# Kernel tuning notes

Measured on AMD Instinct MI355X. Metric: run time of the kernel, lower is better.

Reference implementation:

```python
import jax, jax.numpy as jnp
import numpy as np

B, S, D_IN = 16, 512, 768
HID, OUT = 64, 12
NEG = 1e12


def setup_inputs() -> dict:
    key = jax.random.key(0)
    k1, k2, k3 = jax.random.split(key, 3)
    x = jax.random.normal(k1, (B, S, D_IN), dtype=jnp.float32)
    mask = jnp.ones((B, S), dtype=jnp.float32)
    W = jax.random.normal(k2, (D_IN, HID * OUT * 2), dtype=jnp.float32) * 0.02
    b = jax.random.normal(k3, (HID * OUT * 2,), dtype=jnp.float32) * 0.02
    return {"x": x, "mask": mask, "W": W, "b": b}


def reference(x, mask, W, b):
    Bb, Ss, _ = x.shape
    h, out = HID, OUT
    # QKV-style projection, split into `out` heads of 2h each
    proj = (x @ W + b).reshape(Bb, Ss, out, 2 * h)  # [b, s, out, 2h]
    qw, kw = proj[..., :h], proj[..., h:]           # [b, s, out, h]

    # Sinusoidal position embedding (merge='zero'): interleaved sin/cos
    pos_ids = jnp.arange(Ss, dtype=x.dtype)
    inv_freq = jnp.power(10000.0, -2.0 * jnp.arange(h // 2, dtype=x.dtype) / h)
    ang = pos_ids[:, None] * inv_freq               # [s, h/2]
    sin, cos = jnp.sin(ang), jnp.cos(ang)
    # torch: pos[..., None, 1::2].repeat(1,1,1,2) -> TILED (not interleaved)
    cos_pos = jnp.concatenate([cos, cos], axis=-1)[None, :, None, :]  # [1, s, 1, h]
    sin_pos = jnp.concatenate([sin, sin], axis=-1)[None, :, None, :]

    def rope(w):
        # stack([-w_odd, w_even], -1).reshape -> interleaved rotation partner
        w2 = jnp.stack([-w[..., 1::2], w[..., ::2]], axis=-1).reshape(w.shape)
        return w * cos_pos + w2 * sin_pos

    qw = rope(qw)
    kw = rope(kw)

    logits = jnp.einsum('bmhd,bnhd->bhmn', qw, kw)  # [b, out, s, s]

    pad = mask[:, None, None, :]                    # broadcast over [b, out, s, s]
    logits = logits * pad - (1.0 - pad) * NEG

    tril = jnp.tril(jnp.ones((Ss, Ss), dtype=logits.dtype), -1)
    logits = logits - tril * NEG

    return logits / (h ** 0.5)
```

## Files before the change

kernel.cpp:

```cpp
#include <hip/hip_runtime.h>
#include <stdint.h>

#define DIN   768
#define NPROJ 1536
#define SEQ   512
#define NHEAD 12
#define NBATCH 16
#define NEGV  1000000000000.0f

typedef short bf16x8 __attribute__((ext_vector_type(8)));
typedef float f32x4  __attribute__((ext_vector_type(4)));
typedef unsigned short u16x8 __attribute__((ext_vector_type(8)));

__device__ __forceinline__ unsigned short f2bf(float f) {
    union { float f; unsigned int u; } v; v.f = f;
    return (unsigned short)((v.u + 0x7FFFu + ((v.u >> 16) & 1u)) >> 16);
}
__device__ __forceinline__ float bf2f(unsigned short u) {
    union { unsigned int u; float f; } v; v.u = ((unsigned int)u) << 16;
    return v.f;
}

__device__ __forceinline__ void gl_lds16(const unsigned short* g, unsigned short* l) {
    __builtin_amdgcn_global_load_lds(
        (const __attribute__((address_space(1))) unsigned int*)(uintptr_t)g,
        (__attribute__((address_space(3))) unsigned int*)(uintptr_t)l,
        16, 0, 0);
}

__device__ __forceinline__ void stage128x64(const unsigned short* __restrict__ g,
                                            int gstride, unsigned short* lds,
                                            int w, int lane) {
#pragma unroll
    for (int t = 0; t < 4; t++) {
        int lr = w * 32 + t * 8 + (lane >> 3);
        int c16 = (lane & 7) ^ (lr & 7);
        gl_lds16(g + (size_t)lr * gstride + c16 * 8,
                 lds + (w * 32 + t * 8) * 64);
    }
}
__device__ __forceinline__ int swz(int row, int cg) {
    return row * 64 + ((cg ^ (row & 7)) << 3);
}

__global__ __launch_bounds__(256) void k_prep(const float* __restrict__ X,
                                              unsigned short* __restrict__ Xb,
                                              const float* __restrict__ W,
                                              unsigned short* __restrict__ Wt,
                                              float* __restrict__ trig) {
    __shared__ unsigned short T[64][72];
    const int bid = blockIdx.x, tid = threadIdx.x;
    if (bid < 288) {
        int n0 = (bid % 24) * 64, k0 = (bid / 24) * 64;
#pragma unroll
        for (int it = 0; it < 4; it++) {
            int c = tid + it * 256;
            int kl = c >> 4, nl = (c & 15) * 4;
            float4 v = *(const float4*)&W[(size_t)(k0 + kl) * NPROJ + n0 + nl];
            T[nl + 0][kl] = f2bf(v.x);
            T[nl + 1][kl] = f2bf(v.y);
            T[nl + 2][kl] = f2bf(v.z);
            T[nl + 3][kl] = f2bf(v.w);
        }
        __syncthreads();
#pragma unroll
        for (int it = 0; it < 2; it++) {
            int c = tid + it * 256;
            int nl = c >> 3, kb = (c & 7) * 8;
            *(int4*)&Wt[(size_t)(n0 + nl) * DIN + k0 + kb] = *(int4*)&T[nl][kb];
        }
        return;
    }
    if (bid < 352) {
        int gi = (bid - 288) * 256 + tid;
        int ss = gi >> 5, j = gi & 31;
        const float C = 0.41524101186092034f;
        float cs, sn;
        sincosf((float)ss * exp2f(-(float)j * C), &sn, &cs);
        trig[2 * gi]     = cs;
        trig[2 * gi + 1] = sn;
        return;
    }
    int i = ((bid - 352) * 256 + tid) * 4;
    float4 v = *(const float4*)&X[i];
    short4 s;
    s.x = (short)f2bf(v.x); s.y = (short)f2bf(v.y);
    s.z = (short)f2bf(v.z); s.w = (short)f2bf(v.w);
    *(short4*)&Xb[i] = s;
}

template <bool PRE>
__global__ __launch_bounds__(256) void k_gemm(const float* __restrict__ X,
                                              const unsigned short* __restrict__ Xb,
                                              const unsigned short* __restrict__ Wt,
                                              const float* __restrict__ bias,
                                              const float* __restrict__ trig,
                                              unsigned short* __restrict__ P) {
    __shared__ unsigned short smem[17408];
    unsigned short* sA = smem;
    unsigned short* sB = smem + 8192;
    const int tid = threadIdx.x;
    const int bid = blockIdx.x;
    const int xcd = bid & 7, t0 = bid >> 3;
    const int m0 = (xcd + 8 * (t0 / 12)) * 128;
    const int n0 = (t0 % 12) * 128;
    const int lane = tid & 63, w = tid >> 6;
    const int q = lane >> 4, r = lane & 15;
    const int wm = w >> 1, wn = w & 1;
    f32x4 acc[4][4];
#pragma unroll
    for (int i = 0; i < 4; i++)
#pragma unroll
        for (int j = 0; j < 4; j++) acc[i][j] = (f32x4){0.f, 0.f, 0.f, 0.f};

    const unsigned short* Ag = Xb + (size_t)m0 * DIN;
    const unsigned short* Bg = Wt + (size_t)n0 * DIN;

    for (int k0 = 0; k0 < DIN; k0 += 64) {
        __syncthreads();
        if (PRE) {
            stage128x64(Ag + k0, DIN, sA, w, lane);
        } else {
#pragma unroll
            for (int it = 0; it < 4; it++) {
                int c = tid + it * 256;
                int row = c >> 3, c16 = c & 7;
                const float* xp = &X[(size_t)(m0 + row) * DIN + k0 + c16 * 8];
                float4 v0 = *(const float4*)xp;
                float4 v1 = *(const float4*)(xp + 4);
                u16x8 sv;
                sv[0] = f2bf(v0.x); sv[1] = f2bf(v0.y);
                sv[2] = f2bf(v0.z); sv[3] = f2bf(v0.w);
                sv[4] = f2bf(v1.x); sv[5] = f2bf(v1.y);
                sv[6] = f2bf(v1.z); sv[7] = f2bf(v1.w);
                *(u16x8*)&sA[swz(row, c16)] = sv;
            }
        }
        stage128x64(Bg + k0, DIN, sB, w, lane);
        __syncthreads();
#pragma unroll
        for (int kk = 0; kk < 64; kk += 32) {
            const int cg = (kk >> 3) + q;
            bf16x8 af[4], bfr[4];
#pragma unroll
            for (int t = 0; t < 4; t++)
                af[t] = *(const bf16x8*)&sA[swz(wm * 64 + t * 16 + r, cg)];
#pragma unroll
            for (int t = 0; t < 4; t++)
                bfr[t] = *(const bf16x8*)&sB[swz(wn * 64 + t * 16 + r, cg)];
#pragma unroll
            for (int tm = 0; tm < 4; tm++)
#pragma unroll
                for (int tn = 0; tn < 4; tn++)
                    acc[tm][tn] = __builtin_amdgcn_mfma_f32_16x16x32_bf16(
                        af[tm], bfr[tn], acc[tm][tn], 0, 0, 0);
        }
    }
    float bb[4];
#pragma unroll
    for (int tn = 0; tn < 4; tn++) bb[tn] = bias[n0 + wn * 64 + tn * 16 + r];
    __syncthreads();
    unsigned short* sT = smem;
#pragma unroll
    for (int tm = 0; tm < 4; tm++) {
        int rowb = wm * 64 + tm * 16 + q * 4;
#pragma unroll
        for (int tn = 0; tn < 4; tn++) {
            int col = wn * 64 + tn * 16 + r;
#pragma unroll
            for (int i = 0; i < 4; i++)
                sT[(rowb + i) * 136 + col] = f2bf(acc[tm][tn][i] + bb[tn]);
        }
    }
    __syncthreads();
#pragma unroll
    for (int it = 0; it < 8; it++) {
        int c = tid + it * 256;
        int row = c >> 4, colb = (c & 15) * 8;
        int m = m0 + row;
        int s = m & (SEQ - 1);
        int base = colb & 31;
        union { int4 v; unsigned short u[8]; } pk;
        pk.v = *(int4*)&sT[row * 136 + colb];
        float wv[8];
#pragma unroll
        for (int j = 0; j < 8; j++) wv[j] = bf2f(pk.u[j]);
        const float* tp = &trig[2 * (s * 32 + base)];
#pragma unroll
        for (int p = 0; p < 4; p++) {
            float4 tt = *(const float4*)&tp[4 * p];
            float oe = wv[2 * p] * tt.x - wv[2 * p + 1] * tt.y;
            float oo = wv[2 * p + 1] * tt.z + wv[2 * p] * tt.w;
            pk.u[2 * p]     = f2bf(oe);
            pk.u[2 * p + 1] = f2bf(oo);
        }
        *(int4*)&P[(size_t)m * NPROJ + n0 + colb] = pk.v;
    }
}

__global__ __launch_bounds__(256, 2) void k_attn(const unsigned short* __restrict__ P,
                                                 const float* __restrict__ mask,
                                                 float* __restrict__ out) {
    __shared__ __attribute__((aligned(16))) unsigned short smem[32768];
    const int tid = threadIdx.x;
    const int bi = blockIdx.x;
    const int x  = bi & 7, s = bi >> 3;
    const int g  = x + 8 * (s >> 4);
    const int rb = s & 15;
    const int b  = g / NHEAD, h = g % NHEAD;
    const int lane = tid & 63, wn = tid >> 6;
    const int q = lane >> 4, r = lane & 15;
    const int w = wn;
    const size_t obase = ((size_t)((b * NHEAD + h) * SEQ)) * SEQ;
    const int m0 = rb * 32;

    const unsigned short* Pk = P + (size_t)b * SEQ * NPROJ + h * 128 + 64;
#pragma unroll
    for (int c = 0; c < 4; c++)
        stage128x64(Pk + (size_t)(c * 128) * NPROJ, NPROJ, smem + c * 128 * 64, w, lane);

    const unsigned short* Pq = P + (size_t)b * SEQ * NPROJ + h * 128;
    bf16x8 qf[2][2];
#pragma unroll
    for (int rt = 0; rt < 2; rt++)
#pragma unroll
        for (int x2 = 0; x2 < 2; x2++)
            qf[rt][x2] = *(const bf16x8*)
                &Pq[(size_t)(m0 + rt * 16 + r) * NPROJ + x2 * 32 + q * 8];

    f32x4 mk4[8];
#pragma unroll
    for (int t = 0; t < 8; t++)
        mk4[t] = *(const f32x4*)&mask[b * SEQ + (wn * 8 + t) * 16 + q * 4];

    f32x4 acc[8][2];
#pragma unroll
    for (int t = 0; t < 8; t++) {
        acc[t][0] = (f32x4){0.f, 0.f, 0.f, 0.f};
        acc[t][1] = (f32x4){0.f, 0.f, 0.f, 0.f};
    }

    __syncthreads();

#pragma unroll
    for (int t = 0; t < 8; t++) {
        const int ct = wn * 8 + t;
        if (ct >= 2 * rb) {
            bf16x8 kf[2];
#pragma unroll
            for (int x2 = 0; x2 < 2; x2++)
                kf[x2] = *(const bf16x8*)&smem[swz(ct * 16 + r, x2 * 4 + q)];
#pragma unroll
            for (int x2 = 0; x2 < 2; x2++) {
                acc[t][0] = __builtin_amdgcn_mfma_f32_16x16x32_bf16(
                    kf[x2], qf[0][x2], acc[t][0], 0, 0, 0);
                acc[t][1] = __builtin_amdgcn_mfma_f32_16x16x32_bf16(
                    kf[x2], qf[1][x2], acc[t][1], 0, 0, 0);
            }
        }
    }
    __syncthreads();

    float* sOut = (float*)smem;
#pragma unroll
    for (int rt = 0; rt < 2; rt++) {
        const int m = m0 + rt * 16 + r;
#pragma unroll
        for (int t = 0; t < 8; t++) {
            const int ct = wn * 8 + t;
            const int nb = ct * 16 + q * 4;
            f32x4 o;
            if (ct >= 2 * rb) {
#pragma unroll
                for (int j = 0; j < 4; j++)
                    o[j] = (acc[t][rt][j] * mk4[t][j]
                            - (1.f - mk4[t][j]) * NEGV
                            - ((nb + j) < m ? NEGV : 0.f)) * 0.125f;
            } else {
#pragma unroll
                for (int j = 0; j < 4; j++)
                    o[j] = (-(1.f - mk4[t][j]) * NEGV - NEGV) * 0.125f;
            }
            *(f32x4*)&sOut[(rt * 16 + r) * 512 + nb] = o;
        }
    }
    __syncthreads();
    float* od = out + obase + (size_t)m0 * SEQ;
#pragma unroll
    for (int it = 0; it < 16; it++) {
        const int c = tid + it * 256;
        f32x4 v = *(const f32x4*)&sOut[c * 4];
        *(f32x4*)&od[c * 4] = v;
    }
}

extern "C" void kernel_launch(void* const* d_in, const int* in_sizes, int n_in,
                              void* d_out, int out_size, void* d_ws, size_t ws_size,
                              hipStream_t stream) {
    const float* x    = (const float*)d_in[0];
    const float* mask = (const float*)d_in[1];
    const float* W    = (const float*)d_in[2];
    const float* bias = (const float*)d_in[3];
    float* out = (float*)d_out;

    const size_t wtN   = (size_t)NPROJ * DIN;
    const size_t pN    = (size_t)NBATCH * SEQ * NPROJ;
    const size_t xN    = (size_t)NBATCH * SEQ * DIN;
    const size_t trigN = (size_t)SEQ * 32 * 2;
    unsigned short* Wt = (unsigned short*)d_ws;
    unsigned short* P  = Wt + wtN;
    float* trig        = (float*)(P + pN);
    unsigned short* Xb = (unsigned short*)(trig + trigN);
    const bool pre = ws_size >= (wtN + pN + xN) * sizeof(unsigned short)
                               + trigN * sizeof(float);

    const int xblocks = (int)(xN / 1024);
    k_prep<<<pre ? (352 + xblocks) : 352, 256, 0, stream>>>(x, Xb, W, Wt, trig);
    if (pre) {
        k_gemm<true><<<dim3(768), 256, 0, stream>>>(x, Xb, Wt, bias, trig, P);
    } else {
        k_gemm<false><<<dim3(768), 256, 0, stream>>>(x, nullptr, Wt, bias, trig, P);
    }
    k_attn<<<dim3(NBATCH * NHEAD * (SEQ / 32)), 256, 0, stream>>>(P, mask, out);
}
```

Before: 278.8 us.

## Move constant lower-triangle fill into prep kernel and trim attention work

The fully masked strictly-lower-triangular output blocks, which depend only on the mask, are now written by extra blocks appended to the prep kernel. The attention kernel then stores only the upper and diagonal columns of each row block and skips staging K chunks that lie entirely below the diagonal. This takes roughly half of the output writes off the attention kernel's critical path. The cost is a larger prep grid and a variable-width store loop with integer divides.

```diff
diff --git a/kernel.cpp b/kernel.cpp
--- a/kernel.cpp
+++ b/kernel.cpp
@@ -7,6 +7,7 @@
 #define NHEAD 12
 #define NBATCH 16
 #define NEGV  1000000000000.0f
+#define NFILL 2880
 
 typedef short bf16x8 __attribute__((ext_vector_type(8)));
 typedef float f32x4  __attribute__((ext_vector_type(4)));
@@ -47,9 +48,29 @@
                                               unsigned short* __restrict__ Xb,
                                               const float* __restrict__ W,
                                               unsigned short* __restrict__ Wt,
-                                              float* __restrict__ trig) {
+                                              float* __restrict__ trig,
+                                              const float* __restrict__ mask,
+                                              float* __restrict__ out) {
     __shared__ unsigned short T[64][72];
     const int bid = blockIdx.x, tid = threadIdx.x;
+    if (bid >= (int)gridDim.x - NFILL) {
+        int f = bid - ((int)gridDim.x - NFILL);
+        int g = f / 15, rb = f % 15 + 1;
+        int b = g / NHEAD, h = g % NHEAD;
+        const int m0 = rb * 32, W4 = 8 * rb;
+        const size_t obase = ((size_t)((b * NHEAD + h) * SEQ)) * SEQ;
+        for (int i = tid; i < 32 * W4; i += 256) {
+            int row = i / W4, c4 = i - row * W4;
+            int n = c4 * 4;
+            f32x4 mk = *(const f32x4*)&mask[b * SEQ + n];
+            f32x4 o;
+#pragma unroll
+            for (int j = 0; j < 4; j++)
+                o[j] = (-(1.f - mk[j]) * NEGV - NEGV) * 0.125f;
+            *(f32x4*)&out[obase + (size_t)(m0 + row) * SEQ + n] = o;
+        }
+        return;
+    }
     if (bid < 288) {
         int n0 = (bid % 24) * 64, k0 = (bid / 24) * 64;
 #pragma unroll
@@ -217,7 +238,9 @@
     const unsigned short* Pk = P + (size_t)b * SEQ * NPROJ + h * 128 + 64;
 #pragma unroll
     for (int c = 0; c < 4; c++)
-        stage128x64(Pk + (size_t)(c * 128) * NPROJ, NPROJ, smem + c * 128 * 64, w, lane);
+        if ((c + 1) * 128 > m0)
+            stage128x64(Pk + (size_t)(c * 128) * NPROJ, NPROJ,
+                        smem + c * 128 * 64, w, lane);
 
     const unsigned short* Pq = P + (size_t)b * SEQ * NPROJ + h * 128;
     bf16x8 qf[2][2];
@@ -268,29 +291,25 @@
 #pragma unroll
         for (int t = 0; t < 8; t++) {
             const int ct = wn * 8 + t;
+            if (ct < 2 * rb) continue;
             const int nb = ct * 16 + q * 4;
             f32x4 o;
-            if (ct >= 2 * rb) {
-#pragma unroll
-                for (int j = 0; j < 4; j++)
-                    o[j] = (acc[t][rt][j] * mk4[t][j]
-                            - (1.f - mk4[t][j]) * NEGV
-                            - ((nb + j) < m ? NEGV : 0.f)) * 0.125f;
-            } else {
-#pragma unroll
-                for (int j = 0; j < 4; j++)
-                    o[j] = (-(1.f - mk4[t][j]) * NEGV - NEGV) * 0.125f;
-            }
+#pragma unroll
+            for (int j = 0; j < 4; j++)
+                o[j] = (acc[t][rt][j] * mk4[t][j]
+                        - (1.f - mk4[t][j]) * NEGV
+                        - ((nb + j) < m ? NEGV : 0.f)) * 0.125f;
             *(f32x4*)&sOut[(rt * 16 + r) * 512 + nb] = o;
         }
     }
     __syncthreads();
+    const int W4 = 128 - 8 * rb;
     float* od = out + obase + (size_t)m0 * SEQ;
-#pragma unroll
-    for (int it = 0; it < 16; it++) {
-        const int c = tid + it * 256;
-        f32x4 v = *(const f32x4*)&sOut[c * 4];
-        *(f32x4*)&od[c * 4] = v;
+    for (int i = tid; i < 32 * W4; i += 256) {
+        int row = i / W4, c4 = i - row * W4;
+        int n = m0 + c4 * 4;
+        f32x4 v = *(const f32x4*)&sOut[row * 512 + n];
+        *(f32x4*)&od[(size_t)row * SEQ + n] = v;
     }
 }
 
@@ -315,7 +334,8 @@
                                + trigN * sizeof(float);
 
     const int xblocks = (int)(xN / 1024);
-    k_prep<<<pre ? (352 + xblocks) : 352, 256, 0, stream>>>(x, Xb, W, Wt, trig);
+    const int prep_grid = (pre ? (352 + xblocks) : 352) + NFILL;
+    k_prep<<<prep_grid, 256, 0, stream>>>(x, Xb, W, Wt, trig, mask, out);
     if (pre) {
         k_gemm<true><<<dim3(768), 256, 0, stream>>>(x, Xb, Wt, bias, trig, P);
     } else {
```

New measurement: 287.9 us. +3.3%, slower.
